# Performance work log

Measured on AMD Instinct MI355X. Metric: run time of the kernel, lower is better.

## Reference

```python
import jax, jax.numpy as jnp
import numpy as np

WS = 14      # window_size
NH = 12      # num_heads


def setup_inputs() -> dict:
    key = jax.random.key(0)
    k0, k1, k2 = jax.random.split(key, 3)
    B, H, W, C = 8, 56, 56, 768
    x = jax.random.normal(k0, (B, H * W, C), jnp.float32)
    s = 1.0 / np.sqrt(C).astype(np.float32)
    w_qkv = jax.random.normal(k1, (C, 3 * C), jnp.float32) * s   # qkv_bias=False
    w_proj = jax.random.normal(k2, (C, C), jnp.float32) * s
    b_proj = jnp.zeros((C,), jnp.float32)
    return {"x": x, "w_qkv": w_qkv, "w_proj": w_proj, "b_proj": b_proj, "H": H, "W": W}


def reference(x, w_qkv, w_proj, b_proj, H, W):
    ws, nh = WS, NH
    B, N, C = x.shape
    hd = C // nh
    H_ = -(-H // ws) * ws
    W_ = -(-W // ws) * ws
    Hn, Wn = H_ // ws, W_ // ws
    L, N_ = Hn * Wn, ws * ws

    qkv = x @ w_qkv                                   # [B, N, 3C]
    qkv = qkv.reshape(B, H, W, 3 * C)
    # pad AFTER the linear, as in the torch code (padded positions have qkv == 0)
    qkv = jnp.pad(qkv, ((0, 0), (0, H_ - H), (0, W_ - W), (0, 0)))
    # window partition: [B,Hn,ws,Wn,ws,3,nh,hd] -> [3,B,L,nh,N_,hd]
    qkv = qkv.reshape(B, Hn, ws, Wn, ws, 3, nh, hd)
    qkv = qkv.transpose(5, 0, 1, 3, 6, 2, 4, 7).reshape(3, B, L, nh, N_, hd)
    q, k, v = qkv[0], qkv[1], qkv[2]

    scale = hd ** -0.5
    attn = jnp.einsum('blhnd,blhmd->blhnm', q * scale, k)   # [B,L,nh,N_,N_]
    attn = jax.nn.softmax(attn, axis=-1)
    out = jnp.einsum('blhnm,blhmd->blhnd', attn, v)          # [B,L,nh,N_,hd]

    # fold windows back: -> [B,H_,W_,C], crop, flatten
    out = out.reshape(B, Hn, Wn, nh, ws, ws, hd)
    out = out.transpose(0, 1, 4, 2, 5, 3, 6).reshape(B, H_, W_, C)
    out = out[:, :H, :W].reshape(B, N, C)
    return out @ w_proj + b_proj
```

## Files before the change

kernel.cpp:

```cpp
#include <hip/hip_runtime.h>

typedef unsigned short u16;
typedef __attribute__((ext_vector_type(8))) __bf16 bf16x8;
typedef __attribute__((ext_vector_type(4))) float floatx4;

__device__ inline float bf2f(u16 u) {
  union { unsigned u; float f; } v; v.u = ((unsigned)u) << 16; return v.f;
}
__device__ inline u16 f2bf(float f) {
  union { float f; unsigned u; } v; v.f = f;
  unsigned r = v.u + 0x7fffu + ((v.u >> 16) & 1u);
  return (u16)(r >> 16);
}

__device__ inline void glds16(const u16* g, u16* l) {
  __builtin_amdgcn_global_load_lds((const __attribute__((address_space(1))) void*)g,
                                   (__attribute__((address_space(3))) void*)l, 16, 0, 0);
}

__global__ __launch_bounds__(256) void detect_k(const u16* __restrict__ w, int* flag)
{
  __shared__ int cnt;
  if (threadIdx.x == 0) cnt = 0;
  __syncthreads();
  int c = 0;
  for (int i = threadIdx.x; i < 16384; i += 256) {
    const int e = (w[i] >> 7) & 0xFF;
    if (e < 64 || e > 191) ++c;
  }
  atomicAdd(&cnt, c);
  __syncthreads();
  if (threadIdx.x == 0) *flag = (cnt > 256) ? 1 : 0;
}

__global__ __launch_bounds__(256) void cast_x_k(const void* __restrict__ in,
                                                u16* __restrict__ out,
                                                int n4, const int* __restrict__ flag)
{
  const int i = blockIdx.x * 256 + threadIdx.x;
  if (i >= n4) return;
  if (*flag) {
    const float4 v = ((const float4*)in)[i];
    u16 o0 = f2bf(v.x), o1 = f2bf(v.y), o2 = f2bf(v.z), o3 = f2bf(v.w);
    uint2 p; p.x = (unsigned)o0 | ((unsigned)o1 << 16); p.y = (unsigned)o2 | ((unsigned)o3 << 16);
    ((uint2*)out)[i] = p;
  } else {
    ((uint2*)out)[i] = ((const uint2*)in)[i];
  }
}

__global__ __launch_bounds__(256) void ct_transpose_k(const void* __restrict__ in,
                                                      u16* __restrict__ out,
                                                      int R, int C, const int* __restrict__ flag)
{
  __shared__ u16 tile[32][33];
  const int f = *flag;
  const int c0 = blockIdx.x * 32, r0 = blockIdx.y * 32;
  const int tx = threadIdx.x & 31, ty = threadIdx.x >> 5;
#pragma unroll
  for (int i = ty; i < 32; i += 8) {
    const size_t idx = (size_t)(r0 + i) * C + (c0 + tx);
    tile[i][tx] = f ? f2bf(((const float*)in)[idx]) : ((const u16*)in)[idx];
  }
  __syncthreads();
#pragma unroll
  for (int i = ty; i < 32; i += 8)
    out[(size_t)(c0 + i) * R + (r0 + tx)] = tile[tx][i];
}

__global__ __launch_bounds__(256) void bias_cast_k(const void* __restrict__ in,
                                                   float* __restrict__ out,
                                                   int n, const int* __restrict__ flag)
{
  const int i = blockIdx.x * 256 + threadIdx.x;
  if (i >= n) return;
  out[i] = *flag ? ((const float*)in)[i] : bf2f(((const u16*)in)[i]);
}

__global__ __launch_bounds__(256) void gemm_bt(
    const u16* __restrict__ A, const u16* __restrict__ Bt,
    const float* __restrict__ bias, void* __restrict__ C,
    int M, int N, int K, const int* __restrict__ flag, int flagOut, int NT)
{
  __shared__ u16 smem[16384];
  u16* As = smem;
  u16* Bs = smem + 8192;
  const int t = threadIdx.x;
  const int wave = t >> 6, lane = t & 63;
  const int quad = lane >> 4, l15 = lane & 15;
  const int wr = (wave >> 1) << 6, wc = (wave & 1) << 6;

  const int id = blockIdx.x;
  const int grp = id / (14 * NT), rem = id % (14 * NT);
  const int mt = grp * 14 + rem % 14;
  const int ntile = rem / 14;
  const size_t m0 = (size_t)mt * 128;
  const size_t n0 = (size_t)ntile * 128;

  const int srow = wave * 8 + (lane >> 3);
  const int sg = ((lane & 7) ^ (lane >> 3)) * 8;
  const u16* ag = A + (m0 + srow) * (size_t)K + sg;
  const u16* bg = Bt + (n0 + srow) * (size_t)K + sg;
  u16* la = As + wave * 512;
  u16* lb = Bs + wave * 512;

  floatx4 acc[4][4] = {};

  for (int k0 = 0; k0 < K; k0 += 64) {
#pragma unroll
    for (int w = 0; w < 4; ++w) glds16(ag + k0 + (size_t)(w * 32) * K, la + w * 2048);
#pragma unroll
    for (int w = 0; w < 4; ++w) glds16(bg + k0 + (size_t)(w * 32) * K, lb + w * 2048);
    __syncthreads();
#pragma unroll
    for (int ks = 0; ks < 2; ++ks) {
      bf16x8 af[4], bfv[4];
      const int gf = ks * 4 + quad;
      const int slot = (gf ^ (l15 & 7)) * 8;
#pragma unroll
      for (int i = 0; i < 4; ++i)
        af[i] = *(const bf16x8*)(As + (wr + i * 16 + l15) * 64 + slot);
#pragma unroll
      for (int j = 0; j < 4; ++j)
        bfv[j] = *(const bf16x8*)(Bs + (wc + j * 16 + l15) * 64 + slot);
#pragma unroll
      for (int i = 0; i < 4; ++i)
#pragma unroll
        for (int j = 0; j < 4; ++j)
          acc[i][j] = __builtin_amdgcn_mfma_f32_16x16x32_bf16(af[i], bfv[j], acc[i][j], 0, 0, 0);
    }
    __syncthreads();
  }

  float bvj[4];
#pragma unroll
  for (int j = 0; j < 4; ++j)
    bvj[j] = bias ? bias[n0 + wc + j * 16 + l15] : 0.0f;

  if (flagOut && (*flag)) {
    float* scrf = (float*)smem + wave * 576;
    float* Cf = (float*)C;
#pragma unroll
    for (int i = 0; i < 4; ++i)
#pragma unroll
      for (int jp = 0; jp < 2; ++jp) {
#pragma unroll
        for (int jj = 0; jj < 2; ++jj)
#pragma unroll
          for (int r = 0; r < 4; ++r)
            scrf[(quad * 4 + r) * 36 + jj * 16 + l15] = acc[i][jp * 2 + jj][r] + bvj[jp * 2 + jj];
#pragma unroll
        for (int u = lane; u < 128; u += 64) {
          const int row = u >> 3, gr = u & 7;
          float4 vv = *(const float4*)(scrf + row * 36 + gr * 4);
          *(float4*)(Cf + (m0 + wr + i * 16 + row) * (size_t)N + n0 + wc + jp * 32 + gr * 4) = vv;
        }
      }
  } else {
    u16* scr = smem + wave * 1152;
    u16* Cb = (u16*)C;
#pragma unroll
    for (int i = 0; i < 4; ++i) {
#pragma unroll
      for (int j = 0; j < 4; ++j)
#pragma unroll
        for (int r = 0; r < 4; ++r)
          scr[(quad * 4 + r) * 72 + j * 16 + l15] = f2bf(acc[i][j][r] + bvj[j]);
#pragma unroll
      for (int u = lane; u < 128; u += 64) {
        const int row = u >> 3, gr = u & 7;
        int4 vv = *(const int4*)(scr + row * 72 + gr * 8);
        *(int4*)(Cb + (m0 + wr + i * 16 + row) * (size_t)N + n0 + wc + gr * 8) = vv;
      }
    }
  }
}

__global__ __launch_bounds__(256, 2) void attn_win(
    const u16* __restrict__ qkv, u16* __restrict__ o)
{
  __shared__ u16 Ks[196 * 64];
  __shared__ u16 Vt[64 * 208];
  __shared__ u16 Pb[4][16 * 208];
  __shared__ int gtok[208];

  const int bid = blockIdx.x;
  const int h = bid % 12;
  const int l = (bid / 12) % 16;
  const int b = bid / 192;
  const int wr0 = (l >> 2) * 14, wc0 = (l & 3) * 14;
  const int baseTok = b * 3136;

  const int t = threadIdx.x, wave = t >> 6, lane = t & 63;
  const int quad = lane >> 4, l15 = lane & 15;

  if (t < 208) {
    const int nn = t < 196 ? t : 195;
    gtok[t] = baseTok + (wr0 + nn / 14) * 56 + wc0 + nn % 14;
  }
  __syncthreads();

  for (int u = t; u < 196 * 8; u += 256) {
    const int row = u >> 3, gg = u & 7;
    int4 kv = *(const int4*)(qkv + (size_t)gtok[row] * 2304 + 768 + h * 64 + gg * 8);
    *(int4*)(Ks + (row * 8 + (gg ^ (row & 7))) * 8) = kv;
  }
  for (int u = t; u < 208 * 8; u += 256) {
    const int n = u >> 3, dg = u & 7;
    int4 vv = {0, 0, 0, 0};
    if (n < 196)
      vv = *(const int4*)(qkv + (size_t)gtok[n] * 2304 + 1536 + h * 64 + dg * 8);
    const u16* pv = (const u16*)&vv;
#pragma unroll
    for (int j = 0; j < 8; ++j) Vt[(dg * 8 + j) * 208 + n] = pv[j];
  }
  __syncthreads();

  u16* Pw = &Pb[wave][0];
  const bf16x8 zerov = {};

  for (int rt = wave; rt < 13; rt += 4) {
    const int n0r = rt * 16;
    int qn = n0r + l15; if (qn > 195) qn = 195;
    const u16* qrow = qkv + (size_t)gtok[qn] * 2304 + h * 64;
    const bf16x8 aq0 = *(const bf16x8*)(qrow + quad * 8);
    const bf16x8 aq1 = *(const bf16x8*)(qrow + 32 + quad * 8);

    floatx4 s[13];
#pragma unroll
    for (int ct = 0; ct < 13; ++ct) {
      int kr = ct * 16 + l15; if (kr > 195) kr = 195;
      const bf16x8 bk0 = *(const bf16x8*)(Ks + (kr * 8 + (quad ^ (kr & 7))) * 8);
      const bf16x8 bk1 = *(const bf16x8*)(Ks + (kr * 8 + ((quad + 4) ^ (kr & 7))) * 8);
      floatx4 z = {};
      z = __builtin_amdgcn_mfma_f32_16x16x32_bf16(aq0, bk0, z, 0, 0, 0);
      z = __builtin_amdgcn_mfma_f32_16x16x32_bf16(aq1, bk1, z, 0, 0, 0);
      s[ct] = z;
    }

    float mx[4], sm[4];
#pragma unroll
    for (int r = 0; r < 4; ++r) mx[r] = -3e38f;
#pragma unroll
    for (int ct = 0; ct < 13; ++ct) {
      const bool maskct = (ct == 12) && (l15 >= 4);
#pragma unroll
      for (int r = 0; r < 4; ++r) {
        float v = s[ct][r] * 0.125f;
        if (maskct) v = -3e38f;
        s[ct][r] = v;
        mx[r] = fmaxf(mx[r], v);
      }
    }
#pragma unroll
    for (int r = 0; r < 4; ++r)
      for (int off = 1; off < 16; off <<= 1)
        mx[r] = fmaxf(mx[r], __shfl_xor(mx[r], off, 64));
#pragma unroll
    for (int r = 0; r < 4; ++r) sm[r] = 0.0f;
#pragma unroll
    for (int ct = 0; ct < 13; ++ct)
#pragma unroll
      for (int r = 0; r < 4; ++r) {
        const float p = __expf(s[ct][r] - mx[r]);
        s[ct][r] = p;
        sm[r] += p;
      }
#pragma unroll
    for (int r = 0; r < 4; ++r)
      for (int off = 1; off < 16; off <<= 1)
        sm[r] += __shfl_xor(sm[r], off, 64);

#pragma unroll
    for (int ct = 0; ct < 13; ++ct)
#pragma unroll
      for (int r = 0; r < 4; ++r)
        Pw[(quad * 4 + r) * 208 + ct * 16 + l15] = f2bf(s[ct][r]);

    floatx4 oacc[4] = {};
#pragma unroll
    for (int ks = 0; ks < 6; ++ks) {
      const bf16x8 ap = *(const bf16x8*)(Pw + l15 * 208 + ks * 32 + quad * 8);
#pragma unroll
      for (int nt = 0; nt < 4; ++nt) {
        const bf16x8 bv = *(const bf16x8*)(Vt + (nt * 16 + l15) * 208 + ks * 32 + quad * 8);
        oacc[nt] = __builtin_amdgcn_mfma_f32_16x16x32_bf16(ap, bv, oacc[nt], 0, 0, 0);
      }
    }
    {
      const int off = 192 + (quad & 1) * 8;
      bf16x8 ap = *(const bf16x8*)(Pw + l15 * 208 + off);
      if (quad >= 2) ap = zerov;
#pragma unroll
      for (int nt = 0; nt < 4; ++nt) {
        const bf16x8 bv = *(const bf16x8*)(Vt + (nt * 16 + l15) * 208 + off);
        oacc[nt] = __builtin_amdgcn_mfma_f32_16x16x32_bf16(ap, bv, oacc[nt], 0, 0, 0);
      }
    }

    float rs[4];
#pragma unroll
    for (int r = 0; r < 4; ++r) rs[r] = 1.0f / sm[r];

#pragma unroll
    for (int nt = 0; nt < 4; ++nt)
#pragma unroll
      for (int r = 0; r < 4; ++r)
        Pw[(quad * 4 + r) * 208 + nt * 16 + l15] = f2bf(oacc[nt][r] * rs[r]);
#pragma unroll
    for (int u = lane; u < 128; u += 64) {
      const int row = u >> 3, gr = u & 7;
      const int n = n0r + row;
      if (n < 196) {
        int4 vv = *(const int4*)(Pw + row * 208 + gr * 8);
        *(int4*)(o + (size_t)gtok[n] * 768 + h * 64 + gr * 8) = vv;
      }
    }
  }
}

extern "C" void kernel_launch(void* const* d_in, const int* in_sizes, int n_in,
                              void* d_out, int out_size, void* d_ws, size_t ws_size,
                              hipStream_t stream)
{
  const void* x     = d_in[0];
  const void* wqkv  = d_in[1];
  const void* wproj = d_in[2];
  const void* bproj = d_in[3];

  char* ws = (char*)d_ws;
  int*   flag   = (int*)ws;
  float* bprojF = (float*)(ws + 16);
  u16*   wqkvT  = (u16*)(ws + 4096);
  u16*   wprojT = (u16*)(ws + 3543040);
  u16*   qkvbuf = (u16*)(ws + 4722688);
  u16*   xb     = (u16*)(ws + 120328192);
  u16*   attno  = xb;

  detect_k<<<1, 256, 0, stream>>>((const u16*)wqkv, flag);
  cast_x_k<<<dim3(18816), 256, 0, stream>>>(x, xb, 4816896, flag);
  ct_transpose_k<<<dim3(72, 24), 256, 0, stream>>>(wqkv, wqkvT, 768, 2304, flag);
  ct_transpose_k<<<dim3(24, 24), 256, 0, stream>>>(wproj, wprojT, 768, 768, flag);
  bias_cast_k<<<dim3(3), 256, 0, stream>>>(bproj, bprojF, 768, flag);

  gemm_bt<<<dim3(196 * 18), 256, 0, stream>>>(xb, wqkvT, (const float*)nullptr, qkvbuf,
                                              25088, 2304, 768, flag, 0, 18);
  attn_win<<<dim3(1536), 256, 0, stream>>>(qkvbuf, attno);
  gemm_bt<<<dim3(196 * 6), 256, 0, stream>>>(attno, wprojT, bprojF, d_out,
                                             25088, 768, 768, flag, 1, 6);
}
```

Measured before the change: 402.5 us.

## Replace 128x128 GEMM with 256x256 multi-stage pipelined GEMM with XCD-aware tile mapping

Replaces the single-buffered 128x128 bf16 MFMA GEMM with a 512-thread, 256x256-tile kernel. It uses a four-slot LDS ring with three tiles of global-to-LDS prefetch in flight, explicit vmcnt/lgkmcnt waits, s_setprio around the MFMA bursts and a new swizzled LDS layout. Block indices are remapped so consecutive tiles land on the same XCD, aiming to improve L2 reuse. This is meant to hide global load latency and raise arithmetic intensity per byte loaded. The cost is 128 KB of LDS per block (one block per CU) and far fewer workgroups, which worsens tail effects, especially for the small projection GEMM with 294 blocks.

```diff
diff --git a/kernel.cpp b/kernel.cpp
--- a/kernel.cpp
+++ b/kernel.cpp
@@ -77,100 +77,152 @@
   out[i] = *flag ? ((const float*)in)[i] : bf2f(((const u16*)in)[i]);
 }
 
-__global__ __launch_bounds__(256) void gemm_bt(
+__global__ __launch_bounds__(512) void gemm256(
     const u16* __restrict__ A, const u16* __restrict__ Bt,
     const float* __restrict__ bias, void* __restrict__ C,
-    int M, int N, int K, const int* __restrict__ flag, int flagOut, int NT)
-{
-  __shared__ u16 smem[16384];
-  u16* As = smem;
-  u16* Bs = smem + 8192;
+    int M, int N, int K, const int* __restrict__ flag, int flagOut)
+{
+  __shared__ u16 smem[65536];
   const int t = threadIdx.x;
   const int wave = t >> 6, lane = t & 63;
   const int quad = lane >> 4, l15 = lane & 15;
-  const int wr = (wave >> 1) << 6, wc = (wave & 1) << 6;
-
-  const int id = blockIdx.x;
-  const int grp = id / (14 * NT), rem = id % (14 * NT);
-  const int mt = grp * 14 + rem % 14;
-  const int ntile = rem / 14;
-  const size_t m0 = (size_t)mt * 128;
-  const size_t n0 = (size_t)ntile * 128;
-
-  const int srow = wave * 8 + (lane >> 3);
-  const int sg = ((lane & 7) ^ (lane >> 3)) * 8;
-  const u16* ag = A + (m0 + srow) * (size_t)K + sg;
-  const u16* bg = Bt + (n0 + srow) * (size_t)K + sg;
-  u16* la = As + wave * 512;
-  u16* lb = Bs + wave * 512;
-
-  floatx4 acc[4][4] = {};
-
-  for (int k0 = 0; k0 < K; k0 += 64) {
-#pragma unroll
-    for (int w = 0; w < 4; ++w) glds16(ag + k0 + (size_t)(w * 32) * K, la + w * 2048);
-#pragma unroll
-    for (int w = 0; w < 4; ++w) glds16(bg + k0 + (size_t)(w * 32) * K, lb + w * 2048);
-    __syncthreads();
-#pragma unroll
-    for (int ks = 0; ks < 2; ++ks) {
-      bf16x8 af[4], bfv[4];
-      const int gf = ks * 4 + quad;
-      const int slot = (gf ^ (l15 & 7)) * 8;
-#pragma unroll
-      for (int i = 0; i < 4; ++i)
-        af[i] = *(const bf16x8*)(As + (wr + i * 16 + l15) * 64 + slot);
+  const int wm = wave >> 2, wn = wave & 3;
+
+  const int nwg = gridDim.x;
+  const int q = nwg >> 3, r8 = nwg & 7;
+  const int xcd = blockIdx.x & 7, loc = blockIdx.x >> 3;
+  const int wg = (xcd < r8 ? xcd * (q + 1) : r8 * (q + 1) + (xcd - r8) * q) + loc;
+  const int MT = M >> 8;
+  const int mt = wg % MT, ntile = wg / MT;
+  const size_t m0 = (size_t)mt << 8;
+  const size_t n0 = (size_t)ntile << 8;
+
+  int addrA[8], addrB[4];
+#pragma unroll
+  for (int i = 0; i < 8; ++i) {
+    const int row = wm * 128 + i * 16 + l15;
+    const int hs = (((row & 1) << 2) | quad) ^ ((row >> 1) & 7);
+    addrA[i] = (row >> 1) * 64 + hs * 8;
+  }
+#pragma unroll
+  for (int j = 0; j < 4; ++j) {
+    const int row = wn * 64 + j * 16 + l15;
+    const int hs = (((row & 1) << 2) | quad) ^ ((row >> 1) & 7);
+    addrB[j] = (row >> 1) * 64 + hs * 8;
+  }
+
+  const u16* aSrc[2]; const u16* bSrc[2]; int dstOff[2];
+#pragma unroll
+  for (int p = 0; p < 2; ++p) {
+    const int S = p * 512 + wave * 64 + lane;
+    const int line = S >> 3;
+    const int h = (S & 7) ^ (line & 7);
+    const int row = line * 2 + (h >> 2);
+    const int g = (h & 3) * 8;
+    aSrc[p] = A + (m0 + row) * (size_t)K + g;
+    bSrc[p] = Bt + (n0 + row) * (size_t)K + g;
+    dstOff[p] = p * 4096 + wave * 512;
+  }
+
+  const int NTk = K >> 5;
+  floatx4 acc[8][4] = {};
+
+#pragma unroll
+  for (int pt = 0; pt < 3; ++pt) {
+#pragma unroll
+    for (int p = 0; p < 2; ++p) glds16(aSrc[p] + pt * 32, smem + pt * 8192 + dstOff[p]);
+#pragma unroll
+    for (int p = 0; p < 2; ++p) glds16(bSrc[p] + pt * 32, smem + 32768 + pt * 8192 + dstOff[p]);
+  }
+  asm volatile("s_waitcnt vmcnt(8)" ::: "memory");
+  __builtin_amdgcn_s_barrier();
+
+  for (int kt = 0; kt < NTk; ++kt) {
+    const int rb = kt & 3;
+    const u16* sA = smem + rb * 8192;
+    const u16* sB = smem + 32768 + rb * 8192;
+    const bool pf = (kt + 3 < NTk);
+    const int pre = (kt + 3) * 32;
+    const int pr = (kt + 3) & 3;
+
+    bf16x8 a[4], b[4];
+#pragma unroll
+    for (int i = 0; i < 4; ++i) a[i] = *(const bf16x8*)(sA + addrA[i]);
+#pragma unroll
+    for (int j = 0; j < 4; ++j) b[j] = *(const bf16x8*)(sB + addrB[j]);
+    if (pf) {
+      glds16(aSrc[0] + pre, smem + pr * 8192 + dstOff[0]);
+      glds16(aSrc[1] + pre, smem + pr * 8192 + dstOff[1]);
+    }
+    __builtin_amdgcn_s_barrier();
+    asm volatile("s_waitcnt lgkmcnt(0)");
+    __builtin_amdgcn_s_setprio(1);
+#pragma unroll
+    for (int i = 0; i < 4; ++i)
 #pragma unroll
       for (int j = 0; j < 4; ++j)
-        bfv[j] = *(const bf16x8*)(Bs + (wc + j * 16 + l15) * 64 + slot);
-#pragma unroll
-      for (int i = 0; i < 4; ++i)
-#pragma unroll
-        for (int j = 0; j < 4; ++j)
-          acc[i][j] = __builtin_amdgcn_mfma_f32_16x16x32_bf16(af[i], bfv[j], acc[i][j], 0, 0, 0);
-    }
-    __syncthreads();
+        acc[i][j] = __builtin_amdgcn_mfma_f32_16x16x32_bf16(a[i], b[j], acc[i][j], 0, 0, 0);
+    __builtin_amdgcn_s_setprio(0);
+    __builtin_amdgcn_s_barrier();
+
+#pragma unroll
+    for (int i = 0; i < 4; ++i) a[i] = *(const bf16x8*)(sA + addrA[4 + i]);
+    if (pf) {
+      glds16(bSrc[0] + pre, smem + 32768 + pr * 8192 + dstOff[0]);
+      glds16(bSrc[1] + pre, smem + 32768 + pr * 8192 + dstOff[1]);
+    }
+    __builtin_amdgcn_s_barrier();
+    asm volatile("s_waitcnt lgkmcnt(0)");
+    __builtin_amdgcn_s_setprio(1);
+#pragma unroll
+    for (int i = 0; i < 4; ++i)
+#pragma unroll
+      for (int j = 0; j < 4; ++j)
+        acc[4 + i][j] = __builtin_amdgcn_mfma_f32_16x16x32_bf16(a[i], b[j], acc[4 + i][j], 0, 0, 0);
+    __builtin_amdgcn_s_setprio(0);
+    if (kt < NTk - 3)       asm volatile("s_waitcnt vmcnt(8)" ::: "memory");
+    else if (kt == NTk - 3) asm volatile("s_waitcnt vmcnt(4)" ::: "memory");
+    else if (kt == NTk - 2) asm volatile("s_waitcnt vmcnt(0)" ::: "memory");
+    __builtin_amdgcn_s_barrier();
   }
 
   float bvj[4];
 #pragma unroll
   for (int j = 0; j < 4; ++j)
-    bvj[j] = bias ? bias[n0 + wc + j * 16 + l15] : 0.0f;
+    bvj[j] = bias ? bias[n0 + wn * 64 + j * 16 + l15] : 0.0f;
 
   if (flagOut && (*flag)) {
-    float* scrf = (float*)smem + wave * 576;
+    float* scrf = (float*)smem + wave * 1088;
     float* Cf = (float*)C;
 #pragma unroll
-    for (int i = 0; i < 4; ++i)
-#pragma unroll
-      for (int jp = 0; jp < 2; ++jp) {
-#pragma unroll
-        for (int jj = 0; jj < 2; ++jj)
-#pragma unroll
-          for (int r = 0; r < 4; ++r)
-            scrf[(quad * 4 + r) * 36 + jj * 16 + l15] = acc[i][jp * 2 + jj][r] + bvj[jp * 2 + jj];
-#pragma unroll
-        for (int u = lane; u < 128; u += 64) {
-          const int row = u >> 3, gr = u & 7;
-          float4 vv = *(const float4*)(scrf + row * 36 + gr * 4);
-          *(float4*)(Cf + (m0 + wr + i * 16 + row) * (size_t)N + n0 + wc + jp * 32 + gr * 4) = vv;
-        }
-      }
+    for (int i = 0; i < 8; ++i) {
+#pragma unroll
+      for (int j = 0; j < 4; ++j)
+#pragma unroll
+        for (int rr = 0; rr < 4; ++rr)
+          scrf[(quad * 4 + rr) * 68 + j * 16 + l15] = acc[i][j][rr] + bvj[j];
+#pragma unroll
+      for (int u = lane; u < 256; u += 64) {
+        const int row = u >> 4, gr = u & 15;
+        float4 vv = *(const float4*)(scrf + row * 68 + gr * 4);
+        *(float4*)(Cf + (m0 + wm * 128 + i * 16 + row) * (size_t)N + n0 + wn * 64 + gr * 4) = vv;
+      }
+    }
   } else {
     u16* scr = smem + wave * 1152;
     u16* Cb = (u16*)C;
 #pragma unroll
-    for (int i = 0; i < 4; ++i) {
+    for (int i = 0; i < 8; ++i) {
 #pragma unroll
       for (int j = 0; j < 4; ++j)
 #pragma unroll
-        for (int r = 0; r < 4; ++r)
-          scr[(quad * 4 + r) * 72 + j * 16 + l15] = f2bf(acc[i][j][r] + bvj[j]);
+        for (int rr = 0; rr < 4; ++rr)
+          scr[(quad * 4 + rr) * 72 + j * 16 + l15] = f2bf(acc[i][j][rr] + bvj[j]);
 #pragma unroll
       for (int u = lane; u < 128; u += 64) {
         const int row = u >> 3, gr = u & 7;
         int4 vv = *(const int4*)(scr + row * 72 + gr * 8);
-        *(int4*)(Cb + (m0 + wr + i * 16 + row) * (size_t)N + n0 + wc + gr * 8) = vv;
+        *(int4*)(Cb + (m0 + wm * 128 + i * 16 + row) * (size_t)N + n0 + wn * 64 + gr * 8) = vv;
       }
     }
   }
@@ -343,9 +395,9 @@
   ct_transpose_k<<<dim3(24, 24), 256, 0, stream>>>(wproj, wprojT, 768, 768, flag);
   bias_cast_k<<<dim3(3), 256, 0, stream>>>(bproj, bprojF, 768, flag);
 
-  gemm_bt<<<dim3(196 * 18), 256, 0, stream>>>(xb, wqkvT, (const float*)nullptr, qkvbuf,
-                                              25088, 2304, 768, flag, 0, 18);
+  gemm256<<<dim3(882), 512, 0, stream>>>(xb, wqkvT, (const float*)nullptr, qkvbuf,
+                                         25088, 2304, 768, flag, 0);
   attn_win<<<dim3(1536), 256, 0, stream>>>(qkvbuf, attno);
-  gemm_bt<<<dim3(196 * 6), 256, 0, stream>>>(attno, wprojT, bprojF, d_out,
-                                             25088, 768, 768, flag, 1, 6);
-}
+  gemm256<<<dim3(294), 512, 0, stream>>>(attno, wprojT, bprojF, d_out,
+                                         25088, 768, 768, flag, 1);
+}
```

Measured after the change: 398.1 us. Within noise of the previous version (-1.1%).
